# Kernel optimization log

Hardware: AMD Instinct MI355X
Metric: run time of the kernel (lower is better)

The kernel has to match this reference:

```python
import jax, jax.numpy as jnp
import numpy as np

COUNTS = [1536, 8192, 16384, 24576, 12288, 1024, 512, 512, 256, 128, 128]
OFFS = np.concatenate([[0], np.cumsum(COUNTS)]).astype(int).tolist()
N = OFFS[-1]          # 65536 atoms total, sorted by degree
MAX_DEG = 10
BATCH = 2048          # fixed GraphGather batch size
F_IN = 75
GC = 256
DENSE = 512
N_TASKS = 12
N_CLASSES = 2
BN_EPS = 1e-3         # keras BatchNormalization default epsilon


def _graph_conv(x, deg_adjs, w0, wself, wneigh, b):
    # deepchem GraphConv: per-degree (self @ Wself + sum_neighbors @ Wneigh + b), relu
    outs = [x[OFFS[0]:OFFS[1]] @ w0 + b[0]]  # degree-0 atoms: self transform only
    for d in range(1, MAX_DEG + 1):
        self_atoms = x[OFFS[d]:OFFS[d + 1]]            # [n_d, F]
        neigh = x[deg_adjs[d - 1]].sum(axis=1)         # gather [n_d, d, F] -> sum -> [n_d, F]
        outs.append(self_atoms @ wself[d - 1] + neigh @ wneigh[d - 1] + b[d])
    return jax.nn.relu(jnp.concatenate(outs, axis=0))


def _graph_pool(x, deg_adjs):
    # deepchem GraphPool: elementwise max over {self} U neighbors, per degree
    outs = [x[OFFS[0]:OFFS[1]]]  # degree-0 atoms pass through
    for d in range(1, MAX_DEG + 1):
        self_atoms = x[OFFS[d]:OFFS[d + 1]]
        outs.append(jnp.maximum(self_atoms, x[deg_adjs[d - 1]].max(axis=1)))
    return jnp.concatenate(outs, axis=0)


def _bn(x, g, bta, m, v):
    # inference-mode BatchNormalization (training=False -> moving stats)
    return g * (x - m) * jax.lax.rsqrt(v + BN_EPS) + bta


def setup_inputs():
    key = jax.random.key(0)
    ks = iter(jax.random.split(key, 64))
    inp = {}
    inp["atom_features"] = jax.random.normal(next(ks), (N, F_IN), jnp.float32)
    inp["degree_slice"] = jnp.asarray(
        np.stack([np.array(OFFS[:-1]), np.array(COUNTS)], axis=1), jnp.int32)
    # each molecule gets exactly N/BATCH atoms so no GraphGather segment is empty
    inp["membership"] = jax.random.permutation(
        next(ks), jnp.arange(N, dtype=jnp.int32) % BATCH)
    inp["n_samples"] = BATCH
    for d in range(1, MAX_DEG + 1):
        inp["deg_adj_%d" % d] = jax.random.randint(
            next(ks), (COUNTS[d], d), 0, N, jnp.int32)

    def lin(k, fi, fo):
        return jax.random.normal(k, (fi, fo), jnp.float32) * np.float32(1.0 / np.sqrt(fi))

    for li, fi in [(1, F_IN), (2, GC)]:
        inp["gc%d_w0" % li] = lin(next(ks), fi, GC)
        inp["gc%d_wself" % li] = jnp.stack([lin(next(ks), fi, GC) for _ in range(MAX_DEG)])
        inp["gc%d_wneigh" % li] = jnp.stack([lin(next(ks), fi, GC) for _ in range(MAX_DEG)])
        inp["gc%d_b" % li] = jnp.zeros((MAX_DEG + 1, GC), jnp.float32)
    for bi, dim in [(1, GC), (2, GC), (3, DENSE)]:
        inp["bn%d_gamma" % bi] = jnp.ones((dim,), jnp.float32)
        inp["bn%d_beta" % bi] = jnp.zeros((dim,), jnp.float32)
        inp["bn%d_mean" % bi] = jnp.zeros((dim,), jnp.float32)
        inp["bn%d_var" % bi] = jnp.ones((dim,), jnp.float32)
    inp["dense_w"] = lin(next(ks), GC, DENSE)
    inp["dense_b"] = jnp.zeros((DENSE,), jnp.float32)
    inp["out_w"] = lin(next(ks), 2 * DENSE, N_TASKS * N_CLASSES)
    inp["out_b"] = jnp.zeros((N_TASKS * N_CLASSES,), jnp.float32)
    return inp


def reference(atom_features, degree_slice, membership, n_samples,
              deg_adj_1, deg_adj_2, deg_adj_3, deg_adj_4, deg_adj_5,
              deg_adj_6, deg_adj_7, deg_adj_8, deg_adj_9, deg_adj_10,
              gc1_w0, gc1_wself, gc1_wneigh, gc1_b,
              gc2_w0, gc2_wself, gc2_wneigh, gc2_b,
              bn1_gamma, bn1_beta, bn1_mean, bn1_var,
              bn2_gamma, bn2_beta, bn2_mean, bn2_var,
              bn3_gamma, bn3_beta, bn3_mean, bn3_var,
              dense_w, dense_b, out_w, out_b):
    deg_adjs = [deg_adj_1, deg_adj_2, deg_adj_3, deg_adj_4, deg_adj_5,
                deg_adj_6, deg_adj_7, deg_adj_8, deg_adj_9, deg_adj_10]
    h = _graph_conv(atom_features, deg_adjs, gc1_w0, gc1_wself, gc1_wneigh, gc1_b)
    h = _bn(h, bn1_gamma, bn1_beta, bn1_mean, bn1_var)
    h = _graph_pool(h, deg_adjs)
    h = _graph_conv(h, deg_adjs, gc2_w0, gc2_wself, gc2_wneigh, gc2_b)
    h = _bn(h, bn2_gamma, bn2_beta, bn2_mean, bn2_var)
    h = _graph_pool(h, deg_adjs)
    h = jax.nn.relu(h @ dense_w + dense_b)
    h = _bn(h, bn3_gamma, bn3_beta, bn3_mean, bn3_var)
    # GraphGather: tanh(concat(segment_sum, segment_max))
    ssum = jax.ops.segment_sum(h, membership, num_segments=BATCH)
    smax = jax.ops.segment_max(h, membership, num_segments=BATCH)
    fp = jnp.tanh(jnp.concatenate([ssum, smax], axis=1))   # [BATCH, 2*DENSE]
    logits = (fp @ out_w + out_b).reshape(BATCH, N_TASKS, N_CLASSES)[:n_samples]
    probs = jax.nn.softmax(logits, axis=-1)
    return probs, logits, fp
```

## Files before the change

### kernel.cpp

```cpp
#include <hip/hip_runtime.h>
#include <hip/hip_fp16.h>
#include <math.h>

#define NATOMS 65536

typedef _Float16 f16_t;
typedef __attribute__((ext_vector_type(8))) _Float16 half8;
typedef __attribute__((ext_vector_type(4))) float f32x4;

__constant__ int c_offs[12] = {0,1536,9728,26112,50688,62976,64000,64512,65024,65280,65408,65536};

struct Adj { const int* p[10]; };

__device__ __forceinline__ int seg_of(int row) {
    int s = 0;
#pragma unroll
    for (int i = 1; i <= 10; ++i) s += (row >= c_offs[i]) ? 1 : 0;
    return s;
}


__global__ void pack_all(const float* __restrict__ g1w0, const float* __restrict__ g1ws,
                         const float* __restrict__ g1wn,
                         const float* __restrict__ g2w0, const float* __restrict__ g2ws,
                         const float* __restrict__ g2wn,
                         const float* __restrict__ dw, const float* __restrict__ ow,
                         f16_t* __restrict__ W1p, f16_t* __restrict__ W2p,
                         f16_t* __restrict__ Wdp, f16_t* __restrict__ Wop,
                         int* __restrict__ counts) {
    int idx = blockIdx.x * 256 + threadIdx.x;
    if (idx < 2048) counts[idx] = 0;
    if (idx < 540672) {
        int j = idx & 7, lane = (idx >> 3) & 63;
        int kb = (idx >> 9) % 6;
        int rest = idx / (512 * 6);
        int ni = rest & 15, s = rest >> 4;
        int k = kb * 32 + (lane >> 4) * 8 + j;
        int n = ni * 16 + (lane & 15);
        float v = 0.f;
        if (k < 75) v = (s == 0) ? g1w0[k*256 + n] : g1ws[((s-1)*75 + k)*256 + n];
        else if (k >= 96 && k < 171 && s > 0) v = g1wn[((s-1)*75 + (k-96))*256 + n];
        W1p[idx] = (f16_t)v;
    } else if (idx < 1982464) {
        int i2 = idx - 540672;
        int j = i2 & 7, lane = (i2 >> 3) & 63;
        int kb = (i2 >> 9) & 15;
        int rest = i2 >> 13;
        int ni = rest & 15, s = rest >> 4;
        int k = kb * 32 + (lane >> 4) * 8 + j;
        int n = ni * 16 + (lane & 15);
        float v = 0.f;
        if (k < 256) v = (s == 0) ? g2w0[k*256 + n] : g2ws[((s-1)*256 + k)*256 + n];
        else if (s > 0) v = g2wn[((s-1)*256 + (k-256))*256 + n];
        W2p[i2] = (f16_t)v;
    } else if (idx < 2113536) {
        int i2 = idx - 1982464;
        int j = i2 & 7, lane = (i2 >> 3) & 63;
        int kb = (i2 >> 9) & 7;
        int ni = (i2 >> 12) & 31;
        int k = kb * 32 + (lane >> 4) * 8 + j;
        int n = ni * 16 + (lane & 15);
        Wdp[i2] = (f16_t)dw[(size_t)k*512 + n];
    } else {
        int i2 = idx - 2113536;
        int j = i2 & 7, lane = (i2 >> 3) & 63;
        int kb = (i2 >> 9) & 31;
        int ni = i2 >> 14;
        int k = kb * 32 + (lane >> 4) * 8 + j;
        int n = ni * 16 + (lane & 15);
        Wop[i2] = (n < 24) ? (f16_t)ow[k*24 + n] : (f16_t)0.f;
    }
}

__global__ void cvt_pad(const float* __restrict__ xf,
                        f16_t* __restrict__ xq_rm, f16_t* __restrict__ xq_bl) {
    int idx = blockIdx.x * 256 + threadIdx.x;
    int r = idx / 12;
    int cc = idx - r * 12;
    int c = cc << 3;
    f16_t o[8];
#pragma unroll
    for (int e = 0; e < 8; ++e)
        o[e] = (c + e < 75) ? (f16_t)xf[(size_t)r*75 + c + e] : (f16_t)0.f;
    *(uint4*)(xq_rm + (size_t)r*96 + c) = *(uint4*)o;
    *(uint4*)(xq_bl + (size_t)(r>>4)*1536 + (c>>5)*512 + ((c>>3)&3)*128 + (r&15)*8) = *(uint4*)o;
}

template<int D, bool ISMAX, int LD>
__device__ __forceinline__ void gathD(float* v, const f16_t* __restrict__ src,
                                      const int* __restrict__ ap, int c) {
    int rows[D];
#pragma unroll
    for (int j = 0; j < D; ++j) rows[j] = ap[j];
    uint4 raw[D];
#pragma unroll
    for (int j = 0; j < D; ++j) raw[j] = *(const uint4*)(src + (size_t)rows[j]*LD + c);
#pragma unroll
    for (int j = 0; j < D; ++j) {
        const f16_t* u = (const f16_t*)&raw[j];
#pragma unroll
        for (int e = 0; e < 8; ++e) {
            float f = (float)u[e];
            v[e] = ISMAX ? fmaxf(v[e], f) : (v[e] + f);
        }
    }
}

template<bool ISMAX, int LD>
__device__ __forceinline__ void gath_switch(float* v, const f16_t* __restrict__ src,
                                            const int* __restrict__ ap, int s, int c) {
    switch (s) {
        case 1:  gathD<1,ISMAX,LD>(v,src,ap,c);  break;
        case 2:  gathD<2,ISMAX,LD>(v,src,ap,c);  break;
        case 3:  gathD<3,ISMAX,LD>(v,src,ap,c);  break;
        case 4:  gathD<4,ISMAX,LD>(v,src,ap,c);  break;
        case 5:  gathD<5,ISMAX,LD>(v,src,ap,c);  break;
        case 6:  gathD<6,ISMAX,LD>(v,src,ap,c);  break;
        case 7:  gathD<7,ISMAX,LD>(v,src,ap,c);  break;
        case 8:  gathD<8,ISMAX,LD>(v,src,ap,c);  break;
        case 9:  gathD<9,ISMAX,LD>(v,src,ap,c);  break;
        case 10: gathD<10,ISMAX,LD>(v,src,ap,c); break;
        default: break;
    }
}

__global__ __launch_bounds__(256) void nbsum_x(const f16_t* __restrict__ xq_rm,
                                               f16_t* __restrict__ NBX, Adj adj) {
    int idx = blockIdx.x * 256 + threadIdx.x;
    int r = idx >> 4;
    int cc = idx & 15;
    if (cc >= 12) return;
    int c = cc << 3;
    int s = seg_of(r);
    float v[8];
#pragma unroll
    for (int e = 0; e < 8; ++e) v[e] = 0.f;
    if (s > 0)
        gath_switch<false,96>(v, xq_rm, adj.p[s-1] + (size_t)(r - c_offs[s]) * s, s, c);
    f16_t o[8];
#pragma unroll
    for (int e = 0; e < 8; ++e) o[e] = (f16_t)v[e];
    *(uint4*)(NBX + (size_t)(r>>4)*1536 + (c>>5)*512 + ((c>>3)&3)*128 + (r&15)*8) = *(uint4*)o;
}

template<bool DUAL>
__global__ __launch_bounds__(256) void pool_k(const f16_t* __restrict__ H,
                                              f16_t* __restrict__ P_bl,
                                              f16_t* __restrict__ P_rm, Adj adj) {
    int idx = blockIdx.x * 256 + threadIdx.x;
    int r = idx >> 5;
    int c = (idx & 31) << 3;
    int s = seg_of(r);
    uint4 self = *(const uint4*)(H + (size_t)r*256 + c);
    const f16_t* hp = (const f16_t*)&self;
    float v[8];
#pragma unroll
    for (int e = 0; e < 8; ++e) v[e] = (float)hp[e];
    if (s > 0)
        gath_switch<true,256>(v, H, adj.p[s-1] + (size_t)(r - c_offs[s]) * s, s, c);
    f16_t o[8];
#pragma unroll
    for (int e = 0; e < 8; ++e) o[e] = (f16_t)v[e];
    *(uint4*)(P_bl + (size_t)(r>>4)*4096 + (c>>5)*512 + ((c>>3)&3)*128 + (r&15)*8) = *(uint4*)o;
    if (DUAL)
        *(uint4*)(P_rm + (size_t)r*256 + c) = *(uint4*)o;
}

__global__ __launch_bounds__(256) void nbsum_k(const f16_t* __restrict__ P_rm,
                                               f16_t* __restrict__ NB, Adj adj) {
    int idx = blockIdx.x * 256 + threadIdx.x;
    int r = idx >> 5;
    int c = (idx & 31) << 3;
    int s = seg_of(r);
    float v[8];
#pragma unroll
    for (int e = 0; e < 8; ++e) v[e] = 0.f;
    if (s > 0)
        gath_switch<false,256>(v, P_rm, adj.p[s-1] + (size_t)(r - c_offs[s]) * s, s, c);
    f16_t o[8];
#pragma unroll
    for (int e = 0; e < 8; ++e) o[e] = (f16_t)v[e];
    *(uint4*)(NB + (size_t)(r>>4)*4096 + (c>>5)*512 + ((c>>3)&3)*128 + (r&15)*8) = *(uint4*)o;
}

template<int NKB, int KSPB, int NKBA0, int NKBA1, int N, int NY, bool SEG>
__global__ __launch_bounds__(256)
void gemm_mfma(const f16_t* __restrict__ A0, const f16_t* __restrict__ A1,
               const f16_t* __restrict__ Wp,
               const float* __restrict__ bias,
               const float* __restrict__ bng, const float* __restrict__ bnb,
               const float* __restrict__ bnm, const float* __restrict__ bnv,
               f16_t* __restrict__ C)
{
    constexpr int NNT = N / 16;
    __shared__ f16_t eps[64 * 136];

    const int t = threadIdx.x;
    const int lane = t & 63, wave = t >> 6;
    const int wm = wave >> 1, wn = wave & 1;
    const int quad = lane >> 4, l16 = lane & 15;
    const int id = blockIdx.x;
    const int xcd = id & 7;
    const int jj = id >> 3;
    const int xi = jj / NY;
    const int y  = jj - xi * NY;
    const int r0 = (xi * 8 + xcd) * 128;
    const int n0 = y * 128;
    const int seg = SEG ? seg_of(r0) : 0;
    const int nbase = n0 >> 4;
    const int rtg = r0 >> 4;

    f32x4 acc[4][4];
#pragma unroll
    for (int mi = 0; mi < 4; ++mi)
#pragma unroll
        for (int ni = 0; ni < 4; ++ni) acc[mi][ni] = (f32x4){0.f,0.f,0.f,0.f};

    auto loadA = [&](half8* a, int kb) {
        const f16_t* base;
        size_t rstride;
        int kbl;
        if (kb < KSPB) { base = A0; rstride = NKBA0; kbl = kb; }
        else           { base = A1; rstride = NKBA1; kbl = kb - KSPB; }
#pragma unroll
        for (int mi = 0; mi < 4; ++mi)
            a[mi] = *(const half8*)(base + ((size_t)(rtg + wm*4 + mi)*rstride + kbl)*512 + lane*8);
    };
    auto loadB = [&](half8* b, int kb) {
#pragma unroll
        for (int ni = 0; ni < 4; ++ni)
            b[ni] = *(const half8*)(Wp + ((size_t)(seg*NNT + nbase + wn*4 + ni)*NKB + kb)*512 + lane*8);
    };
    auto domfma = [&](half8* a, half8* b) {
#pragma unroll
        for (int mi = 0; mi < 4; ++mi)
#pragma unroll
            for (int ni = 0; ni < 4; ++ni)
                acc[mi][ni] = __builtin_amdgcn_mfma_f32_16x16x32_f16(a[mi], b[ni], acc[mi][ni], 0, 0, 0);
    };

    half8 a0[4], b0[4], a1[4], b1[4];
    loadA(a0, 0); loadB(b0, 0);
#pragma unroll
    for (int kb = 0; kb < NKB; kb += 2) {
        loadA(a1, kb + 1); loadB(b1, kb + 1);
        domfma(a0, b0);
        if (kb + 2 < NKB) { loadA(a0, kb + 2); loadB(b0, kb + 2); }
        domfma(a1, b1);
    }

#pragma unroll
    for (int p = 0; p < 2; ++p) {
        if (p) __syncthreads();
        if (wm == p) {
#pragma unroll
            for (int ni = 0; ni < 4; ++ni) {
                const int lcol = (wn*4 + ni)*16 + l16;
                const int col = n0 + lcol;
                const float scale = bng[col] * rsqrtf(bnv[col] + 1e-3f);
                const float shift = bnb[col] - bnm[col] * scale;
                const float bv = bias[(SEG ? seg*N : 0) + col];
#pragma unroll
                for (int mi = 0; mi < 4; ++mi) {
                    const int lrowb = mi*16 + quad*4;
#pragma unroll
                    for (int r = 0; r < 4; ++r) {
                        float v = acc[mi][ni][r] + bv;
                        v = fmaxf(v, 0.f);
                        v = fmaf(v, scale, shift);
                        eps[(lrowb + r)*136 + lcol] = (f16_t)v;
                    }
                }
            }
        }
        __syncthreads();
#pragma unroll
        for (int it = 0; it < 4; ++it) {
            int row = it*16 + (t >> 4);
            int ch  = t & 15;
            uint4 v = *(const uint4*)&eps[row*136 + ch*8];
            *(uint4*)(C + (size_t)(r0 + p*64 + row)*N + n0 + ch*8) = v;
        }
    }
}

__global__ void scatter_k(const int* __restrict__ mem, int* __restrict__ counts, int* __restrict__ slots) {
    int i = blockIdx.x * 256 + threadIdx.x;
    int s = mem[i];
    int p = atomicAdd(&counts[s], 1);
    if (p < 32) slots[s*32 + p] = i;
}

__global__ __launch_bounds__(64)
void reduce_k(const f16_t* __restrict__ H3, const int* __restrict__ slots,
              float* __restrict__ fp) {
    int s = blockIdx.x, l = threadIdx.x;
    int c = l * 8;
    const int* sl = slots + s*32;
    float sm[8], mx[8];
#pragma unroll
    for (int e = 0; e < 8; ++e) { sm[e] = 0.f; mx[e] = -INFINITY; }
#pragma unroll
    for (int i = 0; i < 32; ++i) {
        int a = sl[i];
        uint4 raw = *(const uint4*)(H3 + (size_t)a*512 + c);
        const f16_t* u = (const f16_t*)&raw;
#pragma unroll
        for (int e = 0; e < 8; ++e) {
            float f = (float)u[e];
            sm[e] += f;
            mx[e] = fmaxf(mx[e], f);
        }
    }
    float o1[8], o2[8];
#pragma unroll
    for (int e = 0; e < 8; ++e) {
        o1[e] = tanhf(sm[e]); o2[e] = tanhf(mx[e]);
    }
    float* fr = fp + (size_t)s*1024;
    *(float4*)(fr + c)       = *(float4*)&o1[0];
    *(float4*)(fr + c + 4)   = *(float4*)&o1[4];
    *(float4*)(fr + 512 + c)     = *(float4*)&o2[0];
    *(float4*)(fr + 512 + c + 4) = *(float4*)&o2[4];
}

__global__ __launch_bounds__(256)
void final_mfma(const float* __restrict__ fp, const f16_t* __restrict__ Wop,
                const float* __restrict__ out_b,
                float* __restrict__ probs, float* __restrict__ logits) {
    const int t = threadIdx.x;
    const int lane = t & 63, wave = t >> 6;
    const int quad = lane >> 4, l16 = lane & 15;
    const int r0 = blockIdx.x * 256 + wave * 64;

    f32x4 acc[4][2];
#pragma unroll
    for (int mi = 0; mi < 4; ++mi)
#pragma unroll
        for (int ni = 0; ni < 2; ++ni) acc[mi][ni] = (f32x4){0.f,0.f,0.f,0.f};

    size_t rowoff[4];
#pragma unroll
    for (int mi = 0; mi < 4; ++mi)
        rowoff[mi] = (size_t)(r0 + mi*16 + l16) * 1024 + quad*8;
    size_t boff[2];
#pragma unroll
    for (int ni = 0; ni < 2; ++ni)
        boff[ni] = (size_t)ni * 32 * 512 + lane*8;

    auto loadA = [&](half8* a, int kb) {
#pragma unroll
        for (int mi = 0; mi < 4; ++mi) {
            const float* src = fp + rowoff[mi] + kb*32;
            float4 u0 = *(const float4*)(src);
            float4 u1 = *(const float4*)(src + 4);
            half8 h;
            h[0] = (f16_t)u0.x; h[1] = (f16_t)u0.y; h[2] = (f16_t)u0.z; h[3] = (f16_t)u0.w;
            h[4] = (f16_t)u1.x; h[5] = (f16_t)u1.y; h[6] = (f16_t)u1.z; h[7] = (f16_t)u1.w;
            a[mi] = h;
        }
    };
    auto loadB = [&](half8* b, int kb) {
#pragma unroll
        for (int ni = 0; ni < 2; ++ni) b[ni] = *(const half8*)(Wop + boff[ni] + (size_t)kb*512);
    };
    auto domfma = [&](half8* a, half8* b) {
#pragma unroll
        for (int mi = 0; mi < 4; ++mi)
#pragma unroll
            for (int ni = 0; ni < 2; ++ni)
                acc[mi][ni] = __builtin_amdgcn_mfma_f32_16x16x32_f16(a[mi], b[ni], acc[mi][ni], 0, 0, 0);
    };

    half8 a0[4], b0[2], a1[4], b1[2];
    loadA(a0, 0); loadB(b0, 0);
#pragma unroll
    for (int kb = 0; kb < 32; kb += 2) {
        loadA(a1, kb + 1); loadB(b1, kb + 1);
        domfma(a0, b0);
        if (kb + 2 < 32) { loadA(a0, kb + 2); loadB(b0, kb + 2); }
        domfma(a1, b1);
    }

#pragma unroll
    for (int ni = 0; ni < 2; ++ni) {
        const int c = ni*16 + l16;
        const bool ok = (c < 24);
        const float bv = ok ? out_b[c] : 0.f;
#pragma unroll
        for (int mi = 0; mi < 4; ++mi) {
#pragma unroll
            for (int r = 0; r < 4; ++r) {
                float lg = acc[mi][ni][r] + bv;
                float lp = __shfl_xor(lg, 1);
                float m = fmaxf(lg, lp);
                float e  = expf(lg - m);
                float ep = expf(lp - m);
                float pr = e / (e + ep);
                if (ok) {
                    int row = r0 + mi*16 + quad*4 + r;
                    logits[(size_t)row*24 + c] = lg;
                    probs[(size_t)row*24 + c]  = pr;
                }
            }
        }
    }
}

extern "C" void kernel_launch(void* const* d_in, const int* in_sizes, int n_in,
                              void* d_out, int out_size, void* d_ws, size_t ws_size,
                              hipStream_t stream) {
    const float* atom       = (const float*)d_in[0];
    const int*   membership = (const int*)  d_in[2];
    Adj adj;
    for (int d = 0; d < 10; ++d) adj.p[d] = (const int*)d_in[4+d];
    const float* gc1_w0     = (const float*)d_in[14];
    const float* gc1_wself  = (const float*)d_in[15];
    const float* gc1_wneigh = (const float*)d_in[16];
    const float* gc1_b      = (const float*)d_in[17];
    const float* gc2_w0     = (const float*)d_in[18];
    const float* gc2_wself  = (const float*)d_in[19];
    const float* gc2_wneigh = (const float*)d_in[20];
    const float* gc2_b      = (const float*)d_in[21];
    const float* bn1g = (const float*)d_in[22]; const float* bn1b = (const float*)d_in[23];
    const float* bn1m = (const float*)d_in[24]; const float* bn1v = (const float*)d_in[25];
    const float* bn2g = (const float*)d_in[26]; const float* bn2b = (const float*)d_in[27];
    const float* bn2m = (const float*)d_in[28]; const float* bn2v = (const float*)d_in[29];
    const float* bn3g = (const float*)d_in[30]; const float* bn3b = (const float*)d_in[31];
    const float* bn3m = (const float*)d_in[32]; const float* bn3v = (const float*)d_in[33];
    const float* dense_w = (const float*)d_in[34];
    const float* dense_b = (const float*)d_in[35];
    const float* out_w   = (const float*)d_in[36];
    const float* out_b   = (const float*)d_in[37];

    f16_t* wsb = (f16_t*)d_ws;
    f16_t* xq_rm = wsb;
    f16_t* xq_bl = wsb + 6291456;
    f16_t* NBX   = wsb + 12582912;
    f16_t* H1b   = wsb + 18874368;
    f16_t* P1rm  = wsb + 35651584;
    f16_t* P1bl  = wsb + 52428800;
    f16_t* NB2b  = wsb + 69206016;
    f16_t* H2b   = H1b;
    f16_t* P2bl  = NB2b;
    f16_t* H3b   = wsb + 35651584;
    f16_t* W1p   = wsb + 85983232;
    f16_t* W2p   = wsb + 86523904;
    f16_t* Wdp   = wsb + 87965696;
    f16_t* Wop   = wsb + 88096768;
    int*  counts = (int*)(wsb + 88129536);
    int*  slots  = counts + 2048;

    float* outp   = (float*)d_out;
    float* probs  = outp;
    float* logits = outp + 49152;
    float* fp     = outp + 98304;

    pack_all<<<8384, 256, 0, stream>>>(gc1_w0, gc1_wself, gc1_wneigh,
                                       gc2_w0, gc2_wself, gc2_wneigh,
                                       dense_w, out_w,
                                       W1p, W2p, Wdp, Wop, counts);

    cvt_pad<<<(NATOMS*12)/256, 256, 0, stream>>>(atom, xq_rm, xq_bl);
    nbsum_x<<<(NATOMS*16)/256, 256, 0, stream>>>(xq_rm, NBX, adj);
    gemm_mfma<6,3,3,3,256,2,true><<<1024, 256, 0, stream>>>(
        xq_bl, NBX, W1p, gc1_b, bn1g, bn1b, bn1m, bn1v, H1b);
    pool_k<true><<<(NATOMS*32)/256, 256, 0, stream>>>(H1b, P1bl, P1rm, adj);

    nbsum_k<<<(NATOMS*32)/256, 256, 0, stream>>>(P1rm, NB2b, adj);
    gemm_mfma<16,8,8,8,256,2,true><<<1024, 256, 0, stream>>>(
        P1bl, NB2b, W2p, gc2_b, bn2g, bn2b, bn2m, bn2v, H2b);
    pool_k<false><<<(NATOMS*32)/256, 256, 0, stream>>>(H2b, P2bl, nullptr, adj);

    gemm_mfma<8,8,8,8,512,4,false><<<2048, 256, 0, stream>>>(
        P2bl, P2bl, Wdp, dense_b, bn3g, bn3b, bn3m, bn3v, H3b);

    scatter_k<<<NATOMS/256, 256, 0, stream>>>(membership, counts, slots);
    reduce_k<<<2048, 64, 0, stream>>>(H3b, slots, fp);

    final_mfma<<<8, 256, 0, stream>>>(fp, Wop, out_b, probs, logits);
}
```

Measured before the change: 392.5 us.

## Stage GEMM operands through LDS with direct global-to-LDS loads, drop blocked duplicate buffers

GEMM kernels now stage A and B tiles into shared memory with global_load_lds DMA instructions instead of loading fragments straight into registers. The conv-layer GEMMs read row-major activations directly, so cvt_pad, nbsum_x, nbsum_k and the first pool_k no longer write a second blocked copy. This cuts redundant writes and workspace size. In exchange it adds two barriers per K-pair with no double buffering, and the row-major A loads are strided and less coalesced than the old blocked layout.

```diff
diff --git a/kernel.cpp b/kernel.cpp
--- a/kernel.cpp
+++ b/kernel.cpp
@@ -19,6 +19,12 @@
     return s;
 }
 
+__device__ __forceinline__ void glds16(const f16_t* g, f16_t* l) {
+    __builtin_amdgcn_global_load_lds(
+        (const __attribute__((address_space(1))) unsigned int*)g,
+        (__attribute__((address_space(3))) unsigned int*)l,
+        16, 0, 0);
+}
 
 __global__ void pack_all(const float* __restrict__ g1w0, const float* __restrict__ g1ws,
                          const float* __restrict__ g1wn,
@@ -72,8 +78,7 @@
     }
 }
 
-__global__ void cvt_pad(const float* __restrict__ xf,
-                        f16_t* __restrict__ xq_rm, f16_t* __restrict__ xq_bl) {
+__global__ void cvt_pad(const float* __restrict__ xf, f16_t* __restrict__ xq) {
     int idx = blockIdx.x * 256 + threadIdx.x;
     int r = idx / 12;
     int cc = idx - r * 12;
@@ -82,8 +87,7 @@
 #pragma unroll
     for (int e = 0; e < 8; ++e)
         o[e] = (c + e < 75) ? (f16_t)xf[(size_t)r*75 + c + e] : (f16_t)0.f;
-    *(uint4*)(xq_rm + (size_t)r*96 + c) = *(uint4*)o;
-    *(uint4*)(xq_bl + (size_t)(r>>4)*1536 + (c>>5)*512 + ((c>>3)&3)*128 + (r&15)*8) = *(uint4*)o;
+    *(uint4*)(xq + (size_t)r*96 + c) = *(uint4*)o;
 }
 
 template<int D, bool ISMAX, int LD>
@@ -124,7 +128,7 @@
     }
 }
 
-__global__ __launch_bounds__(256) void nbsum_x(const f16_t* __restrict__ xq_rm,
+__global__ __launch_bounds__(256) void nbsum_x(const f16_t* __restrict__ xq,
                                                f16_t* __restrict__ NBX, Adj adj) {
     int idx = blockIdx.x * 256 + threadIdx.x;
     int r = idx >> 4;
@@ -136,17 +140,16 @@
 #pragma unroll
     for (int e = 0; e < 8; ++e) v[e] = 0.f;
     if (s > 0)
-        gath_switch<false,96>(v, xq_rm, adj.p[s-1] + (size_t)(r - c_offs[s]) * s, s, c);
+        gath_switch<false,96>(v, xq, adj.p[s-1] + (size_t)(r - c_offs[s]) * s, s, c);
     f16_t o[8];
 #pragma unroll
     for (int e = 0; e < 8; ++e) o[e] = (f16_t)v[e];
-    *(uint4*)(NBX + (size_t)(r>>4)*1536 + (c>>5)*512 + ((c>>3)&3)*128 + (r&15)*8) = *(uint4*)o;
-}
-
-template<bool DUAL>
+    *(uint4*)(NBX + (size_t)r*96 + c) = *(uint4*)o;
+}
+
+template<bool BLOB>
 __global__ __launch_bounds__(256) void pool_k(const f16_t* __restrict__ H,
-                                              f16_t* __restrict__ P_bl,
-                                              f16_t* __restrict__ P_rm, Adj adj) {
+                                              f16_t* __restrict__ P, Adj adj) {
     int idx = blockIdx.x * 256 + threadIdx.x;
     int r = idx >> 5;
     int c = (idx & 31) << 3;
@@ -161,12 +164,13 @@
     f16_t o[8];
 #pragma unroll
     for (int e = 0; e < 8; ++e) o[e] = (f16_t)v[e];
-    *(uint4*)(P_bl + (size_t)(r>>4)*4096 + (c>>5)*512 + ((c>>3)&3)*128 + (r&15)*8) = *(uint4*)o;
-    if (DUAL)
-        *(uint4*)(P_rm + (size_t)r*256 + c) = *(uint4*)o;
-}
-
-__global__ __launch_bounds__(256) void nbsum_k(const f16_t* __restrict__ P_rm,
+    if (BLOB)
+        *(uint4*)(P + (size_t)(r>>4)*4096 + (c>>5)*512 + ((c>>3)&3)*128 + (r&15)*8) = *(uint4*)o;
+    else
+        *(uint4*)(P + (size_t)r*256 + c) = *(uint4*)o;
+}
+
+__global__ __launch_bounds__(256) void nbsum_k(const f16_t* __restrict__ P,
                                                f16_t* __restrict__ NB, Adj adj) {
     int idx = blockIdx.x * 256 + threadIdx.x;
     int r = idx >> 5;
@@ -176,24 +180,27 @@
 #pragma unroll
     for (int e = 0; e < 8; ++e) v[e] = 0.f;
     if (s > 0)
-        gath_switch<false,256>(v, P_rm, adj.p[s-1] + (size_t)(r - c_offs[s]) * s, s, c);
+        gath_switch<false,256>(v, P, adj.p[s-1] + (size_t)(r - c_offs[s]) * s, s, c);
     f16_t o[8];
 #pragma unroll
     for (int e = 0; e < 8; ++e) o[e] = (f16_t)v[e];
-    *(uint4*)(NB + (size_t)(r>>4)*4096 + (c>>5)*512 + ((c>>3)&3)*128 + (r&15)*8) = *(uint4*)o;
-}
-
-template<int NKB, int KSPB, int NKBA0, int NKBA1, int N, int NY, bool SEG>
+    *(uint4*)(NB + (size_t)r*256 + c) = *(uint4*)o;
+}
+
+template<int K, int KSPLIT, int LDA, int N, int NY, bool SEG>
 __global__ __launch_bounds__(256)
-void gemm_mfma(const f16_t* __restrict__ A0, const f16_t* __restrict__ A1,
-               const f16_t* __restrict__ Wp,
-               const float* __restrict__ bias,
-               const float* __restrict__ bng, const float* __restrict__ bnb,
-               const float* __restrict__ bnm, const float* __restrict__ bnv,
-               f16_t* __restrict__ C)
+void gemm_rm(const f16_t* __restrict__ A0, const f16_t* __restrict__ A1,
+             const f16_t* __restrict__ Wp,
+             const float* __restrict__ bias,
+             const float* __restrict__ bng, const float* __restrict__ bnb,
+             const float* __restrict__ bnm, const float* __restrict__ bnv,
+             f16_t* __restrict__ C)
 {
+    constexpr int NKB = K / 32;
     constexpr int NNT = N / 16;
-    __shared__ f16_t eps[64 * 136];
+    __shared__ char smem[32768];
+    f16_t* sm = (f16_t*)smem;
+    f16_t* eps = (f16_t*)smem;
 
     const int t = threadIdx.x;
     const int lane = t & 63, wave = t >> 6;
@@ -208,7 +215,6 @@
     const int n0 = y * 128;
     const int seg = SEG ? seg_of(r0) : 0;
     const int nbase = n0 >> 4;
-    const int rtg = r0 >> 4;
 
     f32x4 acc[4][4];
 #pragma unroll
@@ -216,42 +222,49 @@
 #pragma unroll
         for (int ni = 0; ni < 4; ++ni) acc[mi][ni] = (f32x4){0.f,0.f,0.f,0.f};
 
-    auto loadA = [&](half8* a, int kb) {
-        const f16_t* base;
-        size_t rstride;
-        int kbl;
-        if (kb < KSPB) { base = A0; rstride = NKBA0; kbl = kb; }
-        else           { base = A1; rstride = NKBA1; kbl = kb - KSPB; }
-#pragma unroll
-        for (int mi = 0; mi < 4; ++mi)
-            a[mi] = *(const half8*)(base + ((size_t)(rtg + wm*4 + mi)*rstride + kbl)*512 + lane*8);
-    };
-    auto loadB = [&](half8* b, int kb) {
-#pragma unroll
-        for (int ni = 0; ni < 4; ++ni)
-            b[ni] = *(const half8*)(Wp + ((size_t)(seg*NNT + nbase + wn*4 + ni)*NKB + kb)*512 + lane*8);
-    };
-    auto domfma = [&](half8* a, half8* b) {
-#pragma unroll
-        for (int mi = 0; mi < 4; ++mi)
+    size_t aoff[2];
+#pragma unroll
+    for (int i = 0; i < 2; ++i)
+        aoff[i] = (size_t)(r0 + (wave*2 + i)*16 + l16) * LDA + quad*8;
+    size_t bbase[2];
+#pragma unroll
+    for (int i = 0; i < 2; ++i)
+        bbase[i] = ((size_t)(seg*NNT + nbase + wave*2 + i) * NKB) * 512 + lane*8;
+
+#pragma unroll
+    for (int kbp = 0; kbp < NKB/2; ++kbp) {
+#pragma unroll
+        for (int u = 0; u < 2; ++u) {
+            const int kb = kbp*2 + u;
+            const int kg = kb * 32;
+            const f16_t* Ab = (kg < KSPLIT) ? (A0 + kg) : (A1 + (kg - KSPLIT));
+#pragma unroll
+            for (int i = 0; i < 2; ++i) {
+                glds16(Ab + aoff[i], sm + u*4096 + (wave*2 + i)*512);
+                glds16(Wp + bbase[i] + (size_t)kb*512, sm + 8192 + u*4096 + (wave*2 + i)*512);
+            }
+        }
+        __syncthreads();
+#pragma unroll
+        for (int u = 0; u < 2; ++u) {
+            half8 a[4], b[4];
+#pragma unroll
+            for (int mi = 0; mi < 4; ++mi)
+                a[mi] = *(const half8*)(sm + u*4096 + (wm*4 + mi)*512 + lane*8);
 #pragma unroll
             for (int ni = 0; ni < 4; ++ni)
-                acc[mi][ni] = __builtin_amdgcn_mfma_f32_16x16x32_f16(a[mi], b[ni], acc[mi][ni], 0, 0, 0);
-    };
-
-    half8 a0[4], b0[4], a1[4], b1[4];
-    loadA(a0, 0); loadB(b0, 0);
-#pragma unroll
-    for (int kb = 0; kb < NKB; kb += 2) {
-        loadA(a1, kb + 1); loadB(b1, kb + 1);
-        domfma(a0, b0);
-        if (kb + 2 < NKB) { loadA(a0, kb + 2); loadB(b0, kb + 2); }
-        domfma(a1, b1);
+                b[ni] = *(const half8*)(sm + 8192 + u*4096 + (wn*4 + ni)*512 + lane*8);
+#pragma unroll
+            for (int mi = 0; mi < 4; ++mi)
+#pragma unroll
+                for (int ni = 0; ni < 4; ++ni)
+                    acc[mi][ni] = __builtin_amdgcn_mfma_f32_16x16x32_f16(a[mi], b[ni], acc[mi][ni], 0, 0, 0);
+        }
+        __syncthreads();
     }
 
 #pragma unroll
     for (int p = 0; p < 2; ++p) {
-        if (p) __syncthreads();
         if (wm == p) {
 #pragma unroll
             for (int ni = 0; ni < 4; ++ni) {
@@ -281,6 +294,108 @@
             uint4 v = *(const uint4*)&eps[row*136 + ch*8];
             *(uint4*)(C + (size_t)(r0 + p*64 + row)*N + n0 + ch*8) = v;
         }
+        __syncthreads();
+    }
+}
+
+template<int NKB, int N, int NY>
+__global__ __launch_bounds__(256)
+void gemm_bl(const f16_t* __restrict__ A,
+             const f16_t* __restrict__ Wp,
+             const float* __restrict__ bias,
+             const float* __restrict__ bng, const float* __restrict__ bnb,
+             const float* __restrict__ bnm, const float* __restrict__ bnv,
+             f16_t* __restrict__ C)
+{
+    constexpr int NNT = N / 16;
+    __shared__ char smem[32768];
+    f16_t* sm = (f16_t*)smem;
+    f16_t* eps = (f16_t*)smem;
+
+    const int t = threadIdx.x;
+    const int lane = t & 63, wave = t >> 6;
+    const int wm = wave >> 1, wn = wave & 1;
+    const int quad = lane >> 4, l16 = lane & 15;
+    const int id = blockIdx.x;
+    const int xcd = id & 7;
+    const int jj = id >> 3;
+    const int xi = jj / NY;
+    const int y  = jj - xi * NY;
+    const int r0 = (xi * 8 + xcd) * 128;
+    const int n0 = y * 128;
+    const int nbase = n0 >> 4;
+    const int rtg = r0 >> 4;
+
+    f32x4 acc[4][4];
+#pragma unroll
+    for (int mi = 0; mi < 4; ++mi)
+#pragma unroll
+        for (int ni = 0; ni < 4; ++ni) acc[mi][ni] = (f32x4){0.f,0.f,0.f,0.f};
+
+#pragma unroll
+    for (int kbp = 0; kbp < NKB/2; ++kbp) {
+#pragma unroll
+        for (int u = 0; u < 2; ++u) {
+            const int kb = kbp*2 + u;
+#pragma unroll
+            for (int i = 0; i < 2; ++i) {
+                const int rt = wave*2 + i;
+                glds16(A + ((size_t)(rtg + rt)*NKB + kb)*512 + lane*8, sm + u*4096 + rt*512);
+                glds16(Wp + ((size_t)(nbase + rt)*NKB + kb)*512 + lane*8,
+                       sm + 8192 + u*4096 + rt*512);
+            }
+        }
+        __syncthreads();
+#pragma unroll
+        for (int u = 0; u < 2; ++u) {
+            half8 a[4], b[4];
+#pragma unroll
+            for (int mi = 0; mi < 4; ++mi)
+                a[mi] = *(const half8*)(sm + u*4096 + (wm*4 + mi)*512 + lane*8);
+#pragma unroll
+            for (int ni = 0; ni < 4; ++ni)
+                b[ni] = *(const half8*)(sm + 8192 + u*4096 + (wn*4 + ni)*512 + lane*8);
+#pragma unroll
+            for (int mi = 0; mi < 4; ++mi)
+#pragma unroll
+                for (int ni = 0; ni < 4; ++ni)
+                    acc[mi][ni] = __builtin_amdgcn_mfma_f32_16x16x32_f16(a[mi], b[ni], acc[mi][ni], 0, 0, 0);
+        }
+        __syncthreads();
+    }
+
+#pragma unroll
+    for (int p = 0; p < 2; ++p) {
+        if (wm == p) {
+#pragma unroll
+            for (int ni = 0; ni < 4; ++ni) {
+                const int lcol = (wn*4 + ni)*16 + l16;
+                const int col = n0 + lcol;
+                const float scale = bng[col] * rsqrtf(bnv[col] + 1e-3f);
+                const float shift = bnb[col] - bnm[col] * scale;
+                const float bv = bias[col];
+#pragma unroll
+                for (int mi = 0; mi < 4; ++mi) {
+                    const int lrowb = mi*16 + quad*4;
+#pragma unroll
+                    for (int r = 0; r < 4; ++r) {
+                        float v = acc[mi][ni][r] + bv;
+                        v = fmaxf(v, 0.f);
+                        v = fmaf(v, scale, shift);
+                        eps[(lrowb + r)*136 + lcol] = (f16_t)v;
+                    }
+                }
+            }
+        }
+        __syncthreads();
+#pragma unroll
+        for (int it = 0; it < 4; ++it) {
+            int row = it*16 + (t >> 4);
+            int ch  = t & 15;
+            uint4 v = *(const uint4*)&eps[row*136 + ch*8];
+            *(uint4*)(C + (size_t)(r0 + p*64 + row)*N + n0 + ch*8) = v;
+        }
+        __syncthreads();
     }
 }
 
@@ -434,21 +549,19 @@
     const float* out_b   = (const float*)d_in[37];
 
     f16_t* wsb = (f16_t*)d_ws;
-    f16_t* xq_rm = wsb;
-    f16_t* xq_bl = wsb + 6291456;
-    f16_t* NBX   = wsb + 12582912;
-    f16_t* H1b   = wsb + 18874368;
-    f16_t* P1rm  = wsb + 35651584;
-    f16_t* P1bl  = wsb + 52428800;
-    f16_t* NB2b  = wsb + 69206016;
+    f16_t* xq    = wsb;
+    f16_t* NBX   = wsb + 6291456;
+    f16_t* H1b   = wsb + 12582912;
+    f16_t* P1rm  = wsb + 29360128;
+    f16_t* NB2rm = wsb + 46137344;
     f16_t* H2b   = H1b;
-    f16_t* P2bl  = NB2b;
-    f16_t* H3b   = wsb + 35651584;
-    f16_t* W1p   = wsb + 85983232;
-    f16_t* W2p   = wsb + 86523904;
-    f16_t* Wdp   = wsb + 87965696;
-    f16_t* Wop   = wsb + 88096768;
-    int*  counts = (int*)(wsb + 88129536);
+    f16_t* P2bl  = NB2rm;
+    f16_t* H3b   = H1b;
+    f16_t* W1p   = wsb + 62914560;
+    f16_t* W2p   = wsb + 63455232;
+    f16_t* Wdp   = wsb + 64897024;
+    f16_t* Wop   = wsb + 65028096;
+    int*  counts = (int*)(wsb + 65060864);
     int*  slots  = counts + 2048;
 
     float* outp   = (float*)d_out;
@@ -461,19 +574,19 @@
                                        dense_w, out_w,
                                        W1p, W2p, Wdp, Wop, counts);
 
-    cvt_pad<<<(NATOMS*12)/256, 256, 0, stream>>>(atom, xq_rm, xq_bl);
-    nbsum_x<<<(NATOMS*16)/256, 256, 0, stream>>>(xq_rm, NBX, adj);
-    gemm_mfma<6,3,3,3,256,2,true><<<1024, 256, 0, stream>>>(
-        xq_bl, NBX, W1p, gc1_b, bn1g, bn1b, bn1m, bn1v, H1b);
-    pool_k<true><<<(NATOMS*32)/256, 256, 0, stream>>>(H1b, P1bl, P1rm, adj);
-
-    nbsum_k<<<(NATOMS*32)/256, 256, 0, stream>>>(P1rm, NB2b, adj);
-    gemm_mfma<16,8,8,8,256,2,true><<<1024, 256, 0, stream>>>(
-        P1bl, NB2b, W2p, gc2_b, bn2g, bn2b, bn2m, bn2v, H2b);
-    pool_k<false><<<(NATOMS*32)/256, 256, 0, stream>>>(H2b, P2bl, nullptr, adj);
-
-    gemm_mfma<8,8,8,8,512,4,false><<<2048, 256, 0, stream>>>(
-        P2bl, P2bl, Wdp, dense_b, bn3g, bn3b, bn3m, bn3v, H3b);
+    cvt_pad<<<(NATOMS*12)/256, 256, 0, stream>>>(atom, xq);
+    nbsum_x<<<(NATOMS*16)/256, 256, 0, stream>>>(xq, NBX, adj);
+    gemm_rm<192,96,96,256,2,true><<<1024, 256, 0, stream>>>(
+        xq, NBX, W1p, gc1_b, bn1g, bn1b, bn1m, bn1v, H1b);
+    pool_k<false><<<(NATOMS*32)/256, 256, 0, stream>>>(H1b, P1rm, adj);
+
+    nbsum_k<<<(NATOMS*32)/256, 256, 0, stream>>>(P1rm, NB2rm, adj);
+    gemm_rm<512,256,256,256,2,true><<<1024, 256, 0, stream>>>(
+        P1rm, NB2rm, W2p, gc2_b, bn2g, bn2b, bn2m, bn2v, H2b);
+    pool_k<true><<<(NATOMS*32)/256, 256, 0, stream>>>(H2b, P2bl, adj);
+
+    gemm_bl<8,512,4><<<2048, 256, 0, stream>>>(
+        P2bl, Wdp, dense_b, bn3g, bn3b, bn3m, bn3v, H3b);
 
     scatter_k<<<NATOMS/256, 256, 0, stream>>>(membership, counts, slots);
     reduce_k<<<2048, 64, 0, stream>>>(H3b, slots, fp);
```

Result: faster. 382.0 us (-2.7%).
